# Kernel optimization log

Measured on AMD Instinct MI355X. Metric: run time of the kernel, lower is better.

## Reference

```python
import jax, jax.numpy as jnp
import numpy as np

B, N, K = 2, 16384, 2048
C_BEV, H, W = 256, 128, 128
RADII = (0.4, 0.8)
NSAMPLE = (16, 32)
PC_MIN = (-51.2, -51.2)
VOXEL = (0.1, 0.1)
BEV_STRIDE = 8.0
C_IN = C_BEV + 16 + 16  # bev + two MSG scales (last mlp channel = 16 each)
C_OUT = 128


def setup_inputs() -> dict:
    key = jax.random.key(0)
    ks = jax.random.split(key, 16)
    pxy = jax.random.uniform(ks[0], (B, N, 2), minval=-51.2, maxval=51.2)
    pz = jax.random.uniform(ks[1], (B, N, 1), minval=-5.0, maxval=3.0)
    pf = jax.random.uniform(ks[2], (B, N, 1))
    points = jnp.concatenate([pxy, pz, pf], axis=-1)  # (B, N, 4) [x,y,z,intensity]
    bev = jax.random.normal(ks[3], (B, C_BEV, H, W), dtype=jnp.float32)
    sa_w1 = jax.random.normal(ks[4], (2, 4, 16)) * 0.1
    sa_s1 = 1.0 + 0.1 * jax.random.normal(ks[5], (2, 16))
    sa_b1 = 0.02 * jax.random.normal(ks[6], (2, 16))
    sa_w2 = jax.random.normal(ks[7], (2, 16, 16)) * 0.1
    sa_s2 = 1.0 + 0.1 * jax.random.normal(ks[8], (2, 16))
    sa_b2 = 0.02 * jax.random.normal(ks[9], (2, 16))
    fuse_w = jax.random.normal(ks[10], (C_IN, C_OUT)) * (1.0 / np.sqrt(C_IN))
    fuse_s = 1.0 + 0.1 * jax.random.normal(ks[11], (C_OUT,))
    fuse_b = 0.02 * jax.random.normal(ks[12], (C_OUT,))
    return dict(points=points, bev=bev, sa_w1=sa_w1, sa_s1=sa_s1, sa_b1=sa_b1,
                sa_w2=sa_w2, sa_s2=sa_s2, sa_b2=sa_b2,
                fuse_w=fuse_w, fuse_s=fuse_s, fuse_b=fuse_b)


def _fps(xyz):
    # furthest point sampling starting at index 0, matching pointnet2_stack_utils
    n = xyz.shape[0]
    def step(carry, _):
        dists, far = carry
        d = jnp.sum((xyz - xyz[far]) ** 2, axis=-1)
        dists = jnp.minimum(dists, d)
        return (dists, jnp.argmax(dists)), far
    far0 = jnp.argmax(jnp.zeros((n,), xyz.dtype))  # 0, with argmax's int dtype
    (_, _), idxs = jax.lax.scan(step, (jnp.full((n,), 1e10, xyz.dtype), far0), None, length=K)
    return idxs  # (K,)


def _bilinear(im, x, y):
    # faithful port of bilinear_interpolate_torch: im (H, W, C), x/y (M,)
    h, w = im.shape[0], im.shape[1]
    x0 = jnp.clip(jnp.floor(x).astype(jnp.int32), 0, w - 1)
    x1 = jnp.clip(jnp.floor(x).astype(jnp.int32) + 1, 0, w - 1)
    y0 = jnp.clip(jnp.floor(y).astype(jnp.int32), 0, h - 1)
    y1 = jnp.clip(jnp.floor(y).astype(jnp.int32) + 1, 0, h - 1)
    Ia, Ib, Ic, Id = im[y0, x0], im[y1, x0], im[y0, x1], im[y1, x1]
    x0f, x1f = x0.astype(x.dtype), x1.astype(x.dtype)
    y0f, y1f = y0.astype(y.dtype), y1.astype(y.dtype)
    wa = (x1f - x) * (y1f - y)
    wb = (x1f - x) * (y - y0f)
    wc = (x - x0f) * (y1f - y)
    wd = (x - x0f) * (y - y0f)
    return Ia * wa[:, None] + Ib * wb[:, None] + Ic * wc[:, None] + Id * wd[:, None]


def _group(xyz, feats, new_xyz, d2, radius, ns):
    # ball query: first ns in-radius neighbors (by point index), pad with first hit,
    # zero empty balls -- matches pointnet2 stack QueryAndGroup semantics.
    n = xyz.shape[0]
    mask = d2 < radius * radius  # (K, N)
    keyi = jnp.where(mask, jnp.arange(n, dtype=jnp.int32)[None, :], n)
    idx = jnp.sort(keyi, axis=1)[:, :ns]  # (K, ns) smallest in-radius indices
    valid = idx < n
    idx = jnp.where(valid, idx, idx[:, :1])  # pad with first neighbor
    empty = ~valid[:, 0]
    idx = jnp.where(empty[:, None], 0, idx)
    g = jnp.concatenate([xyz[idx] - new_xyz[:, None, :], feats[idx]], axis=-1)  # use_xyz
    return jnp.where(empty[:, None, None], 0.0, g)  # (K, ns, 4)


def reference(points, bev, sa_w1, sa_s1, sa_b1, sa_w2, sa_s2, sa_b2, fuse_w, fuse_s, fuse_b):
    xyz = points[..., :3]
    pf = points[..., 3:]
    kp_idx = jax.vmap(_fps)(xyz)  # (B, K)
    keypoints = jnp.take_along_axis(xyz, kp_idx[..., None], axis=1)  # (B, K, 3)
    # BEV bilinear interpolation
    x_idx = (keypoints[..., 0] - PC_MIN[0]) / VOXEL[0] / BEV_STRIDE
    y_idx = (keypoints[..., 1] - PC_MIN[1]) / VOXEL[1] / BEV_STRIDE
    bev_hwc = jnp.transpose(bev, (0, 2, 3, 1))  # (B, H, W, C)
    pb = jax.vmap(_bilinear)(bev_hwc, x_idx, y_idx)  # (B, K, C_BEV)
    # raw-point MSG set abstraction
    d2 = jnp.sum((keypoints[:, :, None, :] - xyz[:, None, :, :]) ** 2, axis=-1)  # (B, K, N)
    pooled = []
    for i, (r, ns) in enumerate(zip(RADII, NSAMPLE)):
        g = jax.vmap(lambda x, f, nx, d: _group(x, f, nx, d, r, ns))(xyz, pf, keypoints, d2)
        h = jax.nn.relu(jnp.einsum('bknc,cd->bknd', g, sa_w1[i]) * sa_s1[i] + sa_b1[i])
        h = jax.nn.relu(jnp.einsum('bknc,cd->bknd', h, sa_w2[i]) * sa_s2[i] + sa_b2[i])
        pooled.append(jnp.max(h, axis=2))  # max_pool over ns -> (B, K, 16)
    feat = jnp.concatenate([pb] + pooled, axis=-1).reshape(B * K, C_IN)
    # Linear(no bias) + BN(eval, folded affine) + ReLU
    return jax.nn.relu((feat @ fuse_w) * fuse_s + fuse_b)  # (B*K, C_OUT)
```

## Files before the change

kernel.cpp:

```cpp
#include <hip/hip_runtime.h>

#define B_ 2
#define N_ 16384
#define K_ 2048
#define CBEV 256
#define HH 128
#define WW 128
#define CIN 288
#define COUT 128

typedef float f32x2 __attribute__((ext_vector_type(2)));

template <int CTRL>
__device__ __forceinline__ float dpp_max(float v) {
  int x = __builtin_amdgcn_update_dpp(0, __float_as_int(v), CTRL, 0xf, 0xf, true);
  return fmaxf(v, __int_as_float(x));
}

__global__ __launch_bounds__(1024) void sort_kernel(
    const float4* __restrict__ points, float4* __restrict__ sorted)
{
  const int b = blockIdx.x, t = threadIdx.x, lane = t & 63, wid = t >> 6;
  const float4* pts = points + (size_t)b * N_;
  float4* dst = sorted + (size_t)b * N_;
  __shared__ int hist[1024];
  __shared__ int wsum[16];
  hist[t] = 0;
  __syncthreads();
  int cells[16];
#pragma unroll
  for (int j = 0; j < 16; ++j) {
    float4 p = pts[t * 16 + j];
    int cx = min(max((int)((p.x + 51.2f) * 0.3125f), 0), 31);
    int cy = min(max((int)((p.y + 51.2f) * 0.3125f), 0), 31);
    int mx = cx, my = cy;
    mx = (mx | (mx << 4)) & 0x0F0F; mx = (mx | (mx << 2)) & 0x3333; mx = (mx | (mx << 1)) & 0x5555;
    my = (my | (my << 4)) & 0x0F0F; my = (my | (my << 2)) & 0x3333; my = (my | (my << 1)) & 0x5555;
    int c = mx | (my << 1);
    cells[j] = c;
    atomicAdd(&hist[c], 1);
  }
  __syncthreads();
  int own = hist[t];
  int v = own;
#pragma unroll
  for (int off = 1; off < 64; off <<= 1) {
    int n = __shfl_up(v, off);
    if (lane >= off) v += n;
  }
  if (lane == 63) wsum[wid] = v;
  __syncthreads();
  int base = 0;
  for (int i = 0; i < wid; ++i) base += wsum[i];
  int excl = base + v - own;
  __syncthreads();
  hist[t] = excl;
  __syncthreads();
#pragma unroll
  for (int j = 0; j < 16; ++j) {
    float4 p = pts[t * 16 + j];
    int pos = atomicAdd(&hist[cells[j]], 1);
    dst[pos] = p;
  }
}

#define FPS_T 1024
#define FPS_PPT 16
#define FPS_PAIRS 8

__global__ __launch_bounds__(FPS_T) void fps_kernel(
    const float4* __restrict__ points, const float4* __restrict__ sorted,
    float4* __restrict__ keypts)
{
  const int b = blockIdx.x, t = threadIdx.x, lane = t & 63, wid = t >> 6;
  const float4* sp = sorted + (size_t)b * N_;

  __shared__ f32x2 xp[FPS_PAIRS][FPS_T];
  __shared__ f32x2 yp[FPS_PAIRS][FPS_T];
  __shared__ float sval[2][16];
  __shared__ float4 scoord[2][16];

  f32x2 zz[FPS_PAIRS], dd[FPS_PAIRS];
  float bxmin = 1e30f, bxmax = -1e30f, bymin = 1e30f, bymax = -1e30f;
  float bzmin = 1e30f, bzmax = -1e30f;
  const int base = t * FPS_PPT;
#pragma unroll
  for (int j = 0; j < FPS_PAIRS; ++j) {
    float4 p0 = sp[base + 2 * j];
    float4 p1 = sp[base + 2 * j + 1];
    f32x2 x; x.x = p0.x; x.y = p1.x;
    f32x2 y; y.x = p0.y; y.y = p1.y;
    xp[j][t] = x; yp[j][t] = y;
    zz[j].x = p0.z; zz[j].y = p1.z;
    dd[j].x = 1e10f; dd[j].y = 1e10f;
    bxmin = fminf(bxmin, fminf(p0.x, p1.x)); bxmax = fmaxf(bxmax, fmaxf(p0.x, p1.x));
    bymin = fminf(bymin, fminf(p0.y, p1.y)); bymax = fmaxf(bymax, fmaxf(p0.y, p1.y));
    bzmin = fminf(bzmin, fminf(p0.z, p1.z)); bzmax = fmaxf(bzmax, fmaxf(p0.z, p1.z));
  }
  float tmax = 1e10f;

  float4 q = points[(size_t)b * N_];
  if (t == 0) keypts[(size_t)b * K_] = q;

  for (int it = 1; it < K_; ++it) {
    const int pr = it & 1;
    float dxl = fmaxf(fmaxf(bxmin - q.x, q.x - bxmax), 0.f);
    float dyl = fmaxf(fmaxf(bymin - q.y, q.y - bymax), 0.f);
    float dzl = fmaxf(fmaxf(bzmin - q.z, q.z - bzmax), 0.f);
    float lb = dxl * dxl + dyl * dyl + dzl * dzl;
    bool act = (lb * 0.999999f < tmax);
    if (__any(act)) {
#pragma clang fp contract(off)
      f32x2 qx, qy, qz;
      qx.x = q.x; qx.y = q.x;
      qy.x = q.y; qy.y = q.y;
      qz.x = q.z; qz.y = q.z;
      f32x2 rm; rm.x = -1.f; rm.y = -1.f;
#pragma unroll
      for (int j = 0; j < FPS_PAIRS; ++j) {
        f32x2 dx = xp[j][t] - qx;
        f32x2 dy = yp[j][t] - qy;
        f32x2 dz = zz[j] - qz;
        f32x2 d = dx * dx + dy * dy + dz * dz;
        d = __builtin_elementwise_min(dd[j], d);
        dd[j] = d;
        rm = __builtin_elementwise_max(rm, d);
      }
      tmax = fmaxf(rm.x, rm.y);
      float wred = tmax;
      wred = dpp_max<0x111>(wred);
      wred = dpp_max<0x112>(wred);
      wred = dpp_max<0x114>(wred);
      wred = dpp_max<0x118>(wred);
      wred = dpp_max<0x142>(wred);
      wred = dpp_max<0x143>(wred);
      float wv = __int_as_float(
          __builtin_amdgcn_readlane(__float_as_int(wred), 63));
      unsigned long long mb = __ballot(tmax == wv);
      int src = __ffsll((long long)mb) - 1;
      if (lane == src) {
        int tjoff = 0;
#pragma unroll
        for (int jj = FPS_PAIRS - 1; jj >= 0; --jj) {
          if (dd[jj].y == wv) tjoff = 2 * jj + 1;
          if (dd[jj].x == wv) tjoff = 2 * jj;
        }
        int fidx = (tjoff >> 1) * (FPS_T * 2) + 2 * t + (tjoff & 1);
        float xx = ((const float*)xp)[fidx];
        float yy = ((const float*)yp)[fidx];
        float zs = 0.f;
#pragma unroll
        for (int jj = 0; jj < FPS_PAIRS; ++jj) {
          zs = (tjoff == 2 * jj) ? zz[jj].x : zs;
          zs = (tjoff == 2 * jj + 1) ? zz[jj].y : zs;
        }
        sval[pr][wid] = wv;
        scoord[pr][wid] = make_float4(xx, yy, zs, 0.f);
      }
    } else {
      if (lane == 0) {
        sval[pr][wid] = sval[pr ^ 1][wid];
        scoord[pr][wid] = scoord[pr ^ 1][wid];
      }
    }
    __syncthreads();
    float v = sval[pr][lane & 15];
    float g = v;
    g = dpp_max<0x111>(g);
    g = dpp_max<0x112>(g);
    g = dpp_max<0x114>(g);
    g = dpp_max<0x118>(g);
    float gm = __int_as_float(
        __builtin_amdgcn_readlane(__float_as_int(g), 15));
    unsigned long long mb2 = __ballot(v == gm);
    int ww = (__ffsll((long long)mb2) - 1) & 15;
    q = scoord[pr][ww];
    if (t == 0) keypts[(size_t)b * K_ + it] = q;
  }
}

__global__ __launch_bounds__(256) void bilinear_kernel(
    const float* __restrict__ bev, const float4* __restrict__ keypts,
    float* __restrict__ feat)
{
  const int kb = blockIdx.x;
  const int b = kb >> 11;
  const int c = threadIdx.x;
  float4 kp = keypts[kb];
  float x = __fsub_rn(kp.x, -51.2f); x = x / 0.1f; x = x / 8.0f;
  float y = __fsub_rn(kp.y, -51.2f); y = y / 0.1f; y = y / 8.0f;
  int xf = (int)floorf(x);
  int yf = (int)floorf(y);
  int x0 = min(max(xf, 0), WW - 1);
  int x1 = min(max(xf + 1, 0), WW - 1);
  int y0 = min(max(yf, 0), HH - 1);
  int y1 = min(max(yf + 1, 0), HH - 1);
  float x0f = (float)x0, x1f = (float)x1, y0f = (float)y0, y1f = (float)y1;
  float wa = (x1f - x) * (y1f - y);
  float wb = (x1f - x) * (y - y0f);
  float wc = (x - x0f) * (y1f - y);
  float wd = (x - x0f) * (y - y0f);
  const float* bb = bev + ((size_t)b * CBEV + c) * (HH * WW);
  float Ia = bb[y0 * WW + x0];
  float Ib = bb[y1 * WW + x0];
  float Ic = bb[y0 * WW + x1];
  float Id = bb[y1 * WW + x1];
  float v = Ia * wa + Ib * wb + Ic * wc + Id * wd;
  feat[(size_t)kb * CIN + c] = v;
}

__global__ __launch_bounds__(256) void group_kernel(
    const float4* __restrict__ points, const float4* __restrict__ keypts,
    const float* __restrict__ sa_w1, const float* __restrict__ sa_s1,
    const float* __restrict__ sa_b1, const float* __restrict__ sa_w2,
    const float* __restrict__ sa_s2, const float* __restrict__ sa_b2,
    float* __restrict__ feat)
{
  const int w = threadIdx.x >> 6;
  const int lane = threadIdx.x & 63;
  const int kb = blockIdx.x * 4 + w;
  const int b = kb >> 11;
  const int d = lane & 15;
  __shared__ int l1[4][16];
  __shared__ int l2[4][32];
  const float4* pts = points + (size_t)b * N_;
  float4 kp = keypts[kb];
  const float r2a = (float)(0.4 * 0.4);
  const float r2b = (float)(0.8 * 0.8);
  int c1 = 0, c2 = 0;
  for (int base = 0; base < N_; base += 64) {
    float4 p = pts[base + lane];
    float dx = __fsub_rn(kp.x, p.x);
    float dy = __fsub_rn(kp.y, p.y);
    float dz = __fsub_rn(kp.z, p.z);
    float d2 = __fadd_rn(__fadd_rn(__fmul_rn(dx, dx), __fmul_rn(dy, dy)),
                         __fmul_rn(dz, dz));
    unsigned long long m2 = __ballot(d2 < r2b);
    unsigned long long m1 = __ballot(d2 < r2a);
    unsigned long long below = (lane == 0) ? 0ull : ((~0ull) >> (64 - lane));
    if (c2 < 32 && m2) {
      int pos = c2 + __popcll(m2 & below);
      if (((m2 >> lane) & 1ull) && pos < 32) l2[w][pos] = base + lane;
      c2 += __popcll(m2); if (c2 > 32) c2 = 32;
    }
    if (c1 < 16 && m1) {
      int pos = c1 + __popcll(m1 & below);
      if (((m1 >> lane) & 1ull) && pos < 16) l1[w][pos] = base + lane;
      c1 += __popcll(m1); if (c1 > 16) c1 = 16;
    }
    if (c1 >= 16 && c2 >= 32) break;
  }
  __syncthreads();

  float pooled[2];
#pragma unroll
  for (int br = 0; br < 2; ++br) {
    const int wo1 = br * 64, so1 = br * 16, wo2 = br * 256;
    float w1r[4], w2r[16];
#pragma unroll
    for (int c = 0; c < 4; ++c) w1r[c] = sa_w1[wo1 + c * 16 + d];
#pragma unroll
    for (int c = 0; c < 16; ++c) w2r[c] = sa_w2[wo2 + c * 16 + d];
    float s1d = sa_s1[so1 + d], b1d = sa_b1[so1 + d];
    float s2d = sa_s2[so1 + d], b2d = sa_b2[so1 + d];
    int cnt = (br == 0) ? c1 : c2;
    float vm = -1e30f;
    int n = cnt > 0 ? cnt : 1;
    for (int j = 0; j < n; ++j) {
      float g0 = 0.f, g1 = 0.f, g2 = 0.f, g3 = 0.f;
      if (j < cnt) {
        int pi = (br == 0) ? l1[w][j] : l2[w][j];
        float4 p = pts[pi];
        g0 = p.x - kp.x; g1 = p.y - kp.y; g2 = p.z - kp.z; g3 = p.w;
      }
      float a = g0 * w1r[0] + g1 * w1r[1] + g2 * w1r[2] + g3 * w1r[3];
      float h1 = fmaxf(0.f, fmaf(a, s1d, b1d));
      float a2 = 0.f;
#pragma unroll
      for (int c = 0; c < 16; ++c) a2 = fmaf(__shfl(h1, c), w2r[c], a2);
      float h2 = fmaxf(0.f, fmaf(a2, s2d, b2d));
      vm = fmaxf(vm, h2);
    }
    pooled[br] = vm;
  }
  if (lane < 16) {
    feat[(size_t)kb * CIN + 256 + d] = pooled[0];
    feat[(size_t)kb * CIN + 272 + d] = pooled[1];
  }
}

__global__ __launch_bounds__(128) void fuse_kernel(
    const float* __restrict__ feat, const float* __restrict__ fw,
    const float* __restrict__ fs, const float* __restrict__ fb,
    float* __restrict__ out)
{
  __shared__ float rows[8 * CIN];
  const int d = threadIdx.x;
  const size_t r0 = (size_t)blockIdx.x * 8;
  for (int i = d; i < 8 * CIN; i += 128) rows[i] = feat[r0 * CIN + i];
  __syncthreads();
  float acc[8];
#pragma unroll
  for (int r = 0; r < 8; ++r) acc[r] = 0.f;
  for (int c = 0; c < CIN; ++c) {
    float wv = fw[c * COUT + d];
#pragma unroll
    for (int r = 0; r < 8; ++r) acc[r] = fmaf(rows[r * CIN + c], wv, acc[r]);
  }
  float sd = fs[d], bd = fb[d];
#pragma unroll
  for (int r = 0; r < 8; ++r)
    out[(r0 + r) * COUT + d] = fmaxf(0.f, fmaf(acc[r], sd, bd));
}

extern "C" void kernel_launch(void* const* d_in, const int* in_sizes, int n_in,
                              void* d_out, int out_size, void* d_ws, size_t ws_size,
                              hipStream_t stream) {
  const float4* points = (const float4*)d_in[0];
  const float* bev    = (const float*)d_in[1];
  const float* sa_w1  = (const float*)d_in[2];
  const float* sa_s1  = (const float*)d_in[3];
  const float* sa_b1  = (const float*)d_in[4];
  const float* sa_w2  = (const float*)d_in[5];
  const float* sa_s2  = (const float*)d_in[6];
  const float* sa_b2  = (const float*)d_in[7];
  const float* fuse_w = (const float*)d_in[8];
  const float* fuse_s = (const float*)d_in[9];
  const float* fuse_b = (const float*)d_in[10];
  float* out = (float*)d_out;

  char* ws = (char*)d_ws;
  float* feat = (float*)ws;
  float4* keypts = (float4*)(ws + (size_t)(B_ * K_) * CIN * sizeof(float));
  float4* sorted = (float4*)(ws + (size_t)(B_ * K_) * CIN * sizeof(float)
                                + (size_t)(B_ * K_) * sizeof(float4));

  hipLaunchKernelGGL(sort_kernel, dim3(B_), dim3(1024), 0, stream, points, sorted);
  hipLaunchKernelGGL(fps_kernel, dim3(B_), dim3(FPS_T), 0, stream,
                     points, sorted, keypts);
  hipLaunchKernelGGL(bilinear_kernel, dim3(B_ * K_), dim3(256), 0, stream,
                     bev, keypts, feat);
  hipLaunchKernelGGL(group_kernel, dim3(B_ * K_ / 4), dim3(256), 0, stream,
                     points, keypts, sa_w1, sa_s1, sa_b1, sa_w2, sa_s2, sa_b2, feat);
  hipLaunchKernelGGL(fuse_kernel, dim3(B_ * K_ / 8), dim3(128), 0, stream,
                     feat, fuse_w, fuse_s, fuse_b, out);
}
```

Before: 2.329 ms.

## Keep half of FPS point coordinates in registers and pack the shared reduction slot

The furthest-point-sampling kernel now keeps the x/y coordinates of the first four point pairs per thread in registers. The remaining pairs are stored in LDS as packed float4 (x,y interleaved), so each inner iteration issues fewer LDS reads. The per-wave max value is folded into the w field of the coordinate slot, and the winning coordinates are taken with readlane instead of a second LDS read. A waves_per_eu hint is added to allow the extra register use, which trades more VGPR pressure for less LDS traffic in the serial loop.

```diff
diff --git a/kernel.cpp b/kernel.cpp
--- a/kernel.cpp
+++ b/kernel.cpp
@@ -10,6 +10,7 @@
 #define COUT 128
 
 typedef float f32x2 __attribute__((ext_vector_type(2)));
+typedef float f32x4 __attribute__((ext_vector_type(4)));
 
 template <int CTRL>
 __device__ __forceinline__ float dpp_max(float v) {
@@ -67,19 +68,20 @@
 #define FPS_T 1024
 #define FPS_PPT 16
 #define FPS_PAIRS 8
-
-__global__ __launch_bounds__(FPS_T) void fps_kernel(
+#define REG_PAIRS 4
+
+__global__ __launch_bounds__(FPS_T)
+__attribute__((amdgpu_waves_per_eu(4, 4))) void fps_kernel(
     const float4* __restrict__ points, const float4* __restrict__ sorted,
     float4* __restrict__ keypts)
 {
   const int b = blockIdx.x, t = threadIdx.x, lane = t & 63, wid = t >> 6;
   const float4* sp = sorted + (size_t)b * N_;
 
-  __shared__ f32x2 xp[FPS_PAIRS][FPS_T];
-  __shared__ f32x2 yp[FPS_PAIRS][FPS_T];
-  __shared__ float sval[2][16];
+  __shared__ f32x4 xyq[FPS_PAIRS - REG_PAIRS][FPS_T];
   __shared__ float4 scoord[2][16];
 
+  f32x2 rx[REG_PAIRS], ry[REG_PAIRS];
   f32x2 zz[FPS_PAIRS], dd[FPS_PAIRS];
   float bxmin = 1e30f, bxmax = -1e30f, bymin = 1e30f, bymax = -1e30f;
   float bzmin = 1e30f, bzmax = -1e30f;
@@ -88,9 +90,13 @@
   for (int j = 0; j < FPS_PAIRS; ++j) {
     float4 p0 = sp[base + 2 * j];
     float4 p1 = sp[base + 2 * j + 1];
-    f32x2 x; x.x = p0.x; x.y = p1.x;
-    f32x2 y; y.x = p0.y; y.y = p1.y;
-    xp[j][t] = x; yp[j][t] = y;
+    if (j < REG_PAIRS) {
+      rx[j].x = p0.x; rx[j].y = p1.x;
+      ry[j].x = p0.y; ry[j].y = p1.y;
+    } else {
+      f32x4 v4; v4.x = p0.x; v4.y = p1.x; v4.z = p0.y; v4.w = p1.y;
+      xyq[j - REG_PAIRS][t] = v4;
+    }
     zz[j].x = p0.z; zz[j].y = p1.z;
     dd[j].x = 1e10f; dd[j].y = 1e10f;
     bxmin = fminf(bxmin, fminf(p0.x, p1.x)); bxmax = fmaxf(bxmax, fmaxf(p0.x, p1.x));
@@ -117,9 +123,22 @@
       qz.x = q.z; qz.y = q.z;
       f32x2 rm; rm.x = -1.f; rm.y = -1.f;
 #pragma unroll
-      for (int j = 0; j < FPS_PAIRS; ++j) {
-        f32x2 dx = xp[j][t] - qx;
-        f32x2 dy = yp[j][t] - qy;
+      for (int j = 0; j < REG_PAIRS; ++j) {
+        f32x2 dx = rx[j] - qx;
+        f32x2 dy = ry[j] - qy;
+        f32x2 dz = zz[j] - qz;
+        f32x2 d = dx * dx + dy * dy + dz * dz;
+        d = __builtin_elementwise_min(dd[j], d);
+        dd[j] = d;
+        rm = __builtin_elementwise_max(rm, d);
+      }
+#pragma unroll
+      for (int j = REG_PAIRS; j < FPS_PAIRS; ++j) {
+        f32x4 v4 = xyq[j - REG_PAIRS][t];
+        f32x2 x; x.x = v4.x; x.y = v4.y;
+        f32x2 y; y.x = v4.z; y.y = v4.w;
+        f32x2 dx = x - qx;
+        f32x2 dy = y - qy;
         f32x2 dz = zz[j] - qz;
         f32x2 d = dx * dx + dy * dy + dz * dz;
         d = __builtin_elementwise_min(dd[j], d);
@@ -145,26 +164,34 @@
           if (dd[jj].y == wv) tjoff = 2 * jj + 1;
           if (dd[jj].x == wv) tjoff = 2 * jj;
         }
-        int fidx = (tjoff >> 1) * (FPS_T * 2) + 2 * t + (tjoff & 1);
-        float xx = ((const float*)xp)[fidx];
-        float yy = ((const float*)yp)[fidx];
+        float xx = 0.f, yy = 0.f;
+#pragma unroll
+        for (int jj = 0; jj < REG_PAIRS; ++jj) {
+          xx = (tjoff == 2 * jj) ? rx[jj].x : xx;
+          xx = (tjoff == 2 * jj + 1) ? rx[jj].y : xx;
+          yy = (tjoff == 2 * jj) ? ry[jj].x : yy;
+          yy = (tjoff == 2 * jj + 1) ? ry[jj].y : yy;
+        }
+        if (tjoff >= 2 * REG_PAIRS) {
+          const float* lp = (const float*)&xyq[(tjoff >> 1) - REG_PAIRS][t];
+          int sub = tjoff & 1;
+          xx = lp[sub];
+          yy = lp[2 + sub];
+        }
         float zs = 0.f;
 #pragma unroll
         for (int jj = 0; jj < FPS_PAIRS; ++jj) {
           zs = (tjoff == 2 * jj) ? zz[jj].x : zs;
           zs = (tjoff == 2 * jj + 1) ? zz[jj].y : zs;
         }
-        sval[pr][wid] = wv;
-        scoord[pr][wid] = make_float4(xx, yy, zs, 0.f);
+        scoord[pr][wid] = make_float4(xx, yy, zs, wv);
       }
     } else {
-      if (lane == 0) {
-        sval[pr][wid] = sval[pr ^ 1][wid];
-        scoord[pr][wid] = scoord[pr ^ 1][wid];
-      }
+      if (lane == 0) scoord[pr][wid] = scoord[pr ^ 1][wid];
     }
     __syncthreads();
-    float v = sval[pr][lane & 15];
+    float4 f4 = scoord[pr][lane & 15];
+    float v = f4.w;
     float g = v;
     g = dpp_max<0x111>(g);
     g = dpp_max<0x112>(g);
@@ -173,9 +200,11 @@
     float gm = __int_as_float(
         __builtin_amdgcn_readlane(__float_as_int(g), 15));
     unsigned long long mb2 = __ballot(v == gm);
-    int ww = (__ffsll((long long)mb2) - 1) & 15;
-    q = scoord[pr][ww];
-    if (t == 0) keypts[(size_t)b * K_ + it] = q;
+    int sww = (__ffsll((long long)mb2) - 1) & 15;
+    q.x = __int_as_float(__builtin_amdgcn_readlane(__float_as_int(f4.x), sww));
+    q.y = __int_as_float(__builtin_amdgcn_readlane(__float_as_int(f4.y), sww));
+    q.z = __int_as_float(__builtin_amdgcn_readlane(__float_as_int(f4.z), sww));
+    if (t == 0) keypts[(size_t)b * K_ + it] = make_float4(q.x, q.y, q.z, 0.f);
   }
 }
 
```

New measurement: 2.333 ms. About the same (+0.2%).
